# Kernel tuning notes

Measured on AMD Instinct MI355X. Metric: run time of the kernel, lower is better.

Reference implementation:

```python
import jax, jax.numpy as jnp
import numpy as np

VOCAB = 32000
EMBED = 1024
BATCH = 16384
SEQ = 7


def _convolute(X, kernel):
    # X: (B, L, E); kernel: (h, E) -> (B, L-h+1, E)
    h = kernel.shape[0]
    L = X.shape[1]
    out = X[:, 0:L - h + 1] * kernel[0]
    for t in range(1, h):
        out = out + X[:, t:L - h + 1 + t] * kernel[t]
    return out


def setup_inputs() -> dict:
    key = jax.random.key(0)
    k1, k2, k3, k4, k5, k6 = jax.random.split(key, 6)
    X = jax.random.randint(k1, (BATCH, SEQ), 0, VOCAB)
    emb = jax.random.normal(k2, (VOCAB, EMBED), dtype=jnp.float32)
    conv1 = jax.random.normal(k3, (2, EMBED), dtype=jnp.float32)
    conv2 = jax.random.normal(k4, (2, EMBED), dtype=jnp.float32)
    conv3 = jax.random.normal(k5, (3, EMBED), dtype=jnp.float32)
    conv4 = jax.random.normal(k6, (3, EMBED), dtype=jnp.float32)
    return {"X": X, "emb": emb, "conv1": conv1, "conv2": conv2,
            "conv3": conv3, "conv4": conv4}


def reference(X, emb, conv1, conv2, conv3, conv4):
    H = emb[X]                                  # (B, 7, E)
    H = jax.nn.sigmoid(_convolute(H, conv1))    # (B, 6, E)
    H = jax.nn.sigmoid(_convolute(H, conv2))    # (B, 5, E)
    H = jax.nn.sigmoid(_convolute(H, conv3))    # (B, 3, E)
    H = jax.nn.sigmoid(_convolute(H, conv4))    # (B, 1, E)  (scentence_size == 7)
    return H.reshape(H.shape[0], -1)            # (B, E)
```

## Files before the change

### kernel.cpp

```cpp
#include <hip/hip_runtime.h>


constexpr int EMBED = 1024;
constexpr int SEQ   = 7;
constexpr int ROWS  = 8;

typedef float f2 __attribute__((ext_vector_type(2)));

__device__ __forceinline__ f2 sig2(f2 y) {
    f2 u;
    u.x = __builtin_amdgcn_exp2f(y.x);
    u.y = __builtin_amdgcn_exp2f(y.y);
    f2 d = u + (f2){1.0f, 1.0f};
    f2 r;
    r.x = __builtin_amdgcn_rcpf(d.x);
    r.y = __builtin_amdgcn_rcpf(d.y);
    return r;
}

struct Weights {
    f2 k1[2][2], k2[2][2], k3[3][2], k4[3][2];
};

__device__ __forceinline__ void gather_row(const float* __restrict__ emb,
                                           const int* __restrict__ X,
                                           int row, int e, f2 v[SEQ][2]) {
#pragma unroll
    for (int t = 0; t < SEQ; ++t) {
        const int id = X[row * SEQ + t];
        const float4 f = *(const float4*)(emb + (size_t)id * EMBED + e);
        v[t][0] = (f2){f.x, f.y};
        v[t][1] = (f2){f.z, f.w};
    }
}

__device__ __forceinline__ void compute_row(const f2 v[SEQ][2], const Weights& w,
                                            float* __restrict__ outp) {
    f2 o[2];
#pragma unroll
    for (int p = 0; p < 2; ++p) {
        f2 h1[6];
#pragma unroll
        for (int l = 0; l < 6; ++l)
            h1[l] = sig2(v[l][p] * w.k1[0][p] + v[l + 1][p] * w.k1[1][p]);
        f2 h2[5];
#pragma unroll
        for (int l = 0; l < 5; ++l)
            h2[l] = sig2(h1[l] * w.k2[0][p] + h1[l + 1] * w.k2[1][p]);
        f2 h3[3];
#pragma unroll
        for (int l = 0; l < 3; ++l)
            h3[l] = sig2(h2[l] * w.k3[0][p] + h2[l + 1] * w.k3[1][p] + h2[l + 2] * w.k3[2][p]);
        o[p] = sig2(h3[0] * w.k4[0][p] + h3[1] * w.k4[1][p] + h3[2] * w.k4[2][p]);
    }
    float4 of;
    of.x = o[0].x; of.y = o[0].y; of.z = o[1].x; of.w = o[1].y;
    *(float4*)outp = of;
}

__global__ __launch_bounds__(256, 4) void CSM_62216896250023_kernel(
    const int*   __restrict__ X,
    const float* __restrict__ emb,
    const float* __restrict__ c1,
    const float* __restrict__ c2,
    const float* __restrict__ c3,
    const float* __restrict__ c4,
    float*       __restrict__ out)
{
    const int b0 = blockIdx.x * ROWS;
    const int e  = threadIdx.x << 2;

    const float NL2E = -1.44269504088896f;
    Weights w;
#pragma unroll
    for (int t = 0; t < 2; ++t) {
        float4 f = *(const float4*)(c1 + t * EMBED + e);
        w.k1[t][0] = (f2){f.x * NL2E, f.y * NL2E};
        w.k1[t][1] = (f2){f.z * NL2E, f.w * NL2E};
        f = *(const float4*)(c2 + t * EMBED + e);
        w.k2[t][0] = (f2){f.x * NL2E, f.y * NL2E};
        w.k2[t][1] = (f2){f.z * NL2E, f.w * NL2E};
    }
#pragma unroll
    for (int t = 0; t < 3; ++t) {
        float4 f = *(const float4*)(c3 + t * EMBED + e);
        w.k3[t][0] = (f2){f.x * NL2E, f.y * NL2E};
        w.k3[t][1] = (f2){f.z * NL2E, f.w * NL2E};
        f = *(const float4*)(c4 + t * EMBED + e);
        w.k4[t][0] = (f2){f.x * NL2E, f.y * NL2E};
        w.k4[t][1] = (f2){f.z * NL2E, f.w * NL2E};
    }

    f2 va[SEQ][2], vb[SEQ][2];
    gather_row(emb, X, b0, e, va);
#pragma unroll
    for (int r = 0; r < ROWS; ++r) {
        if (r & 1) {
            if (r + 1 < ROWS) gather_row(emb, X, b0 + r + 1, e, va);
            compute_row(vb, w, out + (size_t)(b0 + r) * EMBED + e);
        } else {
            if (r + 1 < ROWS) gather_row(emb, X, b0 + r + 1, e, vb);
            compute_row(va, w, out + (size_t)(b0 + r) * EMBED + e);
        }
    }
}

extern "C" void kernel_launch(void* const* d_in, const int* in_sizes, int n_in,
                              void* d_out, int out_size, void* d_ws, size_t ws_size,
                              hipStream_t stream) {
    const int*   X   = (const int*)d_in[0];
    const float* emb = (const float*)d_in[1];
    const float* c1  = (const float*)d_in[2];
    const float* c2  = (const float*)d_in[3];
    const float* c3  = (const float*)d_in[4];
    const float* c4  = (const float*)d_in[5];
    float* out = (float*)d_out;

    const int batch = in_sizes[0] / SEQ;
    CSM_62216896250023_kernel<<<batch / ROWS, 256, 0, stream>>>(X, emb, c1, c2, c3, c4, out);
}
```

Measured before the change: 246.3 us.

## Stage conv weights in LDS, preload indices, and use nontemporal output stores

Conv weights are pre-scaled into a 40KB shared-memory buffer and reloaded per layer from LDS instead of held in registers, which frees VGPRs. All token indices for the block's rows are loaded up front. A sched_barrier and an opaque zero offset stop the compiler from hoisting the LDS reads. Output uses nontemporal stores to avoid polluting cache. The cost is extra LDS traffic and a __syncthreads, and 40KB of LDS per block may cap occupancy at 4 blocks per CU.

```diff
diff --git a/kernel.cpp b/kernel.cpp
--- a/kernel.cpp
+++ b/kernel.cpp
@@ -4,8 +4,10 @@
 constexpr int EMBED = 1024;
 constexpr int SEQ   = 7;
 constexpr int ROWS  = 8;
+constexpr int TAPS  = 10;
 
 typedef float f2 __attribute__((ext_vector_type(2)));
+typedef float f4 __attribute__((ext_vector_type(4)));
 
 __device__ __forceinline__ f2 sig2(f2 y) {
     f2 u;
@@ -18,44 +20,61 @@
     return r;
 }
 
-struct Weights {
-    f2 k1[2][2], k2[2][2], k3[3][2], k4[3][2];
-};
-
 __device__ __forceinline__ void gather_row(const float* __restrict__ emb,
-                                           const int* __restrict__ X,
-                                           int row, int e, f2 v[SEQ][2]) {
+                                           const int idx[SEQ],
+                                           int e, f2 v[SEQ][2]) {
 #pragma unroll
     for (int t = 0; t < SEQ; ++t) {
-        const int id = X[row * SEQ + t];
-        const float4 f = *(const float4*)(emb + (size_t)id * EMBED + e);
+        const f4 f = *(const f4*)(emb + (size_t)idx[t] * EMBED + e);
         v[t][0] = (f2){f.x, f.y};
         v[t][1] = (f2){f.z, f.w};
     }
 }
 
-__device__ __forceinline__ void compute_row(const f2 v[SEQ][2], const Weights& w,
-                                            float* __restrict__ outp) {
+__device__ __forceinline__ void ldw(const float* wl, int tap, int e, f2 w[2]) {
+    const f4 f = *(const f4*)(wl + tap * EMBED + e);
+    w[0] = (f2){f.x, f.y};
+    w[1] = (f2){f.z, f.w};
+}
+
+__device__ __forceinline__ void compute_row(const f2 v[SEQ][2], const float* wl,
+                                            int e, float* __restrict__ outp) {
+    f2 wa[2], wb[2], wc[2];
+
+    f2 h1[6][2];
+    ldw(wl, 0, e, wa); ldw(wl, 1, e, wb);
+#pragma unroll
+    for (int l = 0; l < 6; ++l)
+#pragma unroll
+        for (int p = 0; p < 2; ++p)
+            h1[l][p] = sig2(v[l][p] * wa[p] + v[l + 1][p] * wb[p]);
+
+    f2 h2[5][2];
+    ldw(wl, 2, e, wa); ldw(wl, 3, e, wb);
+#pragma unroll
+    for (int l = 0; l < 5; ++l)
+#pragma unroll
+        for (int p = 0; p < 2; ++p)
+            h2[l][p] = sig2(h1[l][p] * wa[p] + h1[l + 1][p] * wb[p]);
+
+    f2 h3[3][2];
+    ldw(wl, 4, e, wa); ldw(wl, 5, e, wb); ldw(wl, 6, e, wc);
+#pragma unroll
+    for (int l = 0; l < 3; ++l)
+#pragma unroll
+        for (int p = 0; p < 2; ++p)
+            h3[l][p] = sig2(h2[l][p] * wa[p] + h2[l + 1][p] * wb[p]
+                            + h2[l + 2][p] * wc[p]);
+
     f2 o[2];
+    ldw(wl, 7, e, wa); ldw(wl, 8, e, wb); ldw(wl, 9, e, wc);
 #pragma unroll
-    for (int p = 0; p < 2; ++p) {
-        f2 h1[6];
-#pragma unroll
-        for (int l = 0; l < 6; ++l)
-            h1[l] = sig2(v[l][p] * w.k1[0][p] + v[l + 1][p] * w.k1[1][p]);
-        f2 h2[5];
-#pragma unroll
-        for (int l = 0; l < 5; ++l)
-            h2[l] = sig2(h1[l] * w.k2[0][p] + h1[l + 1] * w.k2[1][p]);
-        f2 h3[3];
-#pragma unroll
-        for (int l = 0; l < 3; ++l)
-            h3[l] = sig2(h2[l] * w.k3[0][p] + h2[l + 1] * w.k3[1][p] + h2[l + 2] * w.k3[2][p]);
-        o[p] = sig2(h3[0] * w.k4[0][p] + h3[1] * w.k4[1][p] + h3[2] * w.k4[2][p]);
-    }
-    float4 of;
+    for (int p = 0; p < 2; ++p)
+        o[p] = sig2(h3[0][p] * wa[p] + h3[1][p] * wb[p] + h3[2][p] * wc[p]);
+
+    f4 of;
     of.x = o[0].x; of.y = o[0].y; of.z = o[1].x; of.w = o[1].y;
-    *(float4*)outp = of;
+    __builtin_nontemporal_store(of, (f4*)outp);
 }
 
 __global__ __launch_bounds__(256, 4) void CSM_62216896250023_kernel(
@@ -67,41 +86,45 @@
     const float* __restrict__ c4,
     float*       __restrict__ out)
 {
-    const int b0 = blockIdx.x * ROWS;
-    const int e  = threadIdx.x << 2;
+    __shared__ float wlds[TAPS * EMBED];
+
+    const int tid = threadIdx.x;
+    const int e   = tid << 2;
+    const int b0  = blockIdx.x * ROWS;
 
     const float NL2E = -1.44269504088896f;
-    Weights w;
+    {
+        const float* src[TAPS] = {c1, c1 + EMBED,
+                                  c2, c2 + EMBED,
+                                  c3, c3 + EMBED, c3 + 2 * EMBED,
+                                  c4, c4 + EMBED, c4 + 2 * EMBED};
 #pragma unroll
-    for (int t = 0; t < 2; ++t) {
-        float4 f = *(const float4*)(c1 + t * EMBED + e);
-        w.k1[t][0] = (f2){f.x * NL2E, f.y * NL2E};
-        w.k1[t][1] = (f2){f.z * NL2E, f.w * NL2E};
-        f = *(const float4*)(c2 + t * EMBED + e);
-        w.k2[t][0] = (f2){f.x * NL2E, f.y * NL2E};
-        w.k2[t][1] = (f2){f.z * NL2E, f.w * NL2E};
-    }
-#pragma unroll
-    for (int t = 0; t < 3; ++t) {
-        float4 f = *(const float4*)(c3 + t * EMBED + e);
-        w.k3[t][0] = (f2){f.x * NL2E, f.y * NL2E};
-        w.k3[t][1] = (f2){f.z * NL2E, f.w * NL2E};
-        f = *(const float4*)(c4 + t * EMBED + e);
-        w.k4[t][0] = (f2){f.x * NL2E, f.y * NL2E};
-        w.k4[t][1] = (f2){f.z * NL2E, f.w * NL2E};
+        for (int t = 0; t < TAPS; ++t) {
+            f4 f = *(const f4*)(src[t] + e);
+            f *= NL2E;
+            *(f4*)&wlds[t * EMBED + e] = f;
+        }
     }
 
-    f2 va[SEQ][2], vb[SEQ][2];
-    gather_row(emb, X, b0, e, va);
+    int idx[ROWS][SEQ];
+#pragma unroll
+    for (int r = 0; r < ROWS; ++r)
+#pragma unroll
+        for (int t = 0; t < SEQ; ++t)
+            idx[r][t] = X[(b0 + r) * SEQ + t];
+
+    __syncthreads();
+
+    f2 v[2][SEQ][2];
+    gather_row(emb, idx[0], e, v[0]);
 #pragma unroll
     for (int r = 0; r < ROWS; ++r) {
-        if (r & 1) {
-            if (r + 1 < ROWS) gather_row(emb, X, b0 + r + 1, e, va);
-            compute_row(vb, w, out + (size_t)(b0 + r) * EMBED + e);
-        } else {
-            if (r + 1 < ROWS) gather_row(emb, X, b0 + r + 1, e, vb);
-            compute_row(va, w, out + (size_t)(b0 + r) * EMBED + e);
-        }
+        if (r + 1 < ROWS) gather_row(emb, idx[r + 1], e, v[(r + 1) & 1]);
+        __builtin_amdgcn_sched_barrier(0);
+        unsigned rofs = 0;
+        asm volatile("" : "+v"(rofs));
+        compute_row(v[r & 1], (const float*)wlds + rofs, e,
+                    out + (size_t)(b0 + r) * EMBED + e);
     }
 }
 
```

Result: slower. 276.9 us (+12.4%).
